# Performance work log

Measured on AMD Instinct MI355X. Metric: run time of the kernel, lower is better.

The kernel has to match this reference:

```python
import jax, jax.numpy as jnp
import numpy as np

BATCH = 4096
LATENT = 2048
ZDIM = 128
TEMP = 0.5
PRIOR = 0.3
PRIOR_PRIME = 0.5
GAMMA = 1.0
BETA = 0.0
EPS = 1e-8  # torch CosineSimilarity eps


def setup_inputs() -> dict:
    key = jax.random.key(0)
    k = jax.random.split(key, 6)
    return {
        "h_i": jax.random.normal(k[0], (BATCH, LATENT), dtype=jnp.float32),
        "h_j": jax.random.normal(k[1], (BATCH, LATENT), dtype=jnp.float32),
        "z_i": jax.random.normal(k[2], (BATCH, ZDIM), dtype=jnp.float32),
        "z_j": jax.random.normal(k[3], (BATCH, ZDIM), dtype=jnp.float32),
        "target": jax.random.randint(k[4], (BATCH, 1), 0, 2, dtype=jnp.int64 if jax.config.jax_enable_x64 else jnp.int32),
        "W": jax.random.normal(k[5], (1, LATENT), dtype=jnp.float32) * (1.0 / np.sqrt(LATENT)),
        "b": jnp.zeros((1,), dtype=jnp.float32),
        "weight_onnpu": jnp.asarray(0.5, dtype=jnp.float32),
    }


def _onnpu_loss(inp, target):
    # inp: [B, 1] classifier logit; target: [B, 1] in {0, 1} -> {-1, +1}
    t = (target * 2 - 1).astype(inp.dtype)
    positive = (t == 1).astype(inp.dtype)
    unlabeled = (t == -1).astype(inp.dtype)
    one = jnp.asarray(1.0, inp.dtype)
    n_pos = jnp.maximum(one, jnp.sum(positive))
    n_unl = jnp.maximum(one, jnp.sum(unlabeled))
    sig = jax.nn.sigmoid  # loss(x) = sigmoid(-x)
    y_pos = sig(-(positive * inp)) * positive
    y_pos_inv = sig(positive * inp) * positive
    y_unl = sig(unlabeled * inp) * unlabeled
    positive_risk = PRIOR_PRIME / n_pos * jnp.sum(y_pos)
    negative_risk = ((1.0 - PRIOR_PRIME) / (n_unl * (1.0 - PRIOR)) * jnp.sum(y_unl)
                     - (1.0 - PRIOR_PRIME) * PRIOR / (n_pos * (1.0 - PRIOR)) * jnp.sum(y_pos_inv))
    # nnPU correction (nnPU=True, beta=0, gamma=1)
    return jnp.where(negative_risk < -BETA, -GAMMA * negative_risk,
                     positive_risk + negative_risk)


def _nt_xent_loss(z_i, z_j):
    B = z_i.shape[0]
    N = 2 * B
    z = jnp.concatenate([z_i, z_j], axis=0)  # [N, D]
    zn = z / jnp.maximum(jnp.linalg.norm(z, axis=1, keepdims=True), EPS)
    sim = (zn @ zn.T) / TEMP  # [N, N] cosine similarity / temperature
    idx = jnp.arange(N)
    pos = sim[idx, (idx + B) % N]  # positive pair logit per row
    # CE over [positive | all-other-than-self]: denominator is logsumexp over
    # the row with the self-similarity (diagonal) excluded.
    sim_masked = jnp.where(idx[:, None] == idx[None, :], -jnp.inf, sim)
    lse = jax.nn.logsumexp(sim_masked, axis=1)
    return jnp.sum(lse - pos) / N


def reference(h_i, h_j, z_i, z_j, target, W, b, weight_onnpu):
    logit_i = h_i @ W.T + b  # [B, 1]
    logit_j = h_j @ W.T + b
    onnpu_l = 0.5 * (_onnpu_loss(logit_i, target) + _onnpu_loss(logit_j, target))
    nt_xent_l = _nt_xent_loss(z_i, z_j)
    return weight_onnpu * onnpu_l + (1.0 - weight_onnpu) * nt_xent_l
```

## Files before the change

### kernel.cpp

```cpp
#include <hip/hip_runtime.h>

#define BATCH  4096
#define NROWS  8192
#define LATENT 2048
#define ZDIM   128
#define PRIORc       0.3f
#define PRIOR_PRIMEc 0.5f

typedef __attribute__((ext_vector_type(8))) short bf16x8;
typedef __attribute__((ext_vector_type(4))) float f32x4;

__device__ inline unsigned short f2bf_rne(float f) {
    unsigned int u = __float_as_uint(f);
    u = u + 0x7fffu + ((u >> 16) & 1u);
    return (unsigned short)(u >> 16);
}

__device__ inline float wave_reduce_sum(float v) {
#pragma unroll
    for (int m = 1; m < 64; m <<= 1) v += __shfl_xor(v, m, 64);
    return v;
}

__global__ void k_zprep(const float* __restrict__ z_i, const float* __restrict__ z_j,
                        unsigned short* __restrict__ znb, float* __restrict__ pos) {
    int wave = threadIdx.x >> 6, lane = threadIdx.x & 63;
    int r = blockIdx.x * 4 + wave;
    int p = r + BATCH;
    float2 a = ((const float2*)(z_i + (size_t)r * ZDIM))[lane];
    float2 c = ((const float2*)(z_j + (size_t)r * ZDIM))[lane];
    float sa = a.x * a.x + a.y * a.y;
    float sc = c.x * c.x + c.y * c.y;
    float dd = a.x * c.x + a.y * c.y;
    sa = wave_reduce_sum(sa);
    sc = wave_reduce_sum(sc);
    dd = wave_reduce_sum(dd);
    float inva = 1.f / fmaxf(sqrtf(sa), 1e-8f);
    float invc = 1.f / fmaxf(sqrtf(sc), 1e-8f);
    if (lane == 0) {
        float pv = 2.0f * dd * inva * invc;
        pos[r] = pv;
        pos[p] = pv;
    }
    int kt = lane >> 4;
    int q  = (lane >> 2) & 3;
    int j  = (lane & 3) * 2;
    int lrow = q * 16;
    float fa = inva * 1.41421356237f, fc = invc * 1.41421356237f;
    {
        size_t off = ((size_t)((r >> 4) * 4 + kt) * 64 + (lrow + (r & 15))) * 8 + j;
        ushort2 w2; w2.x = f2bf_rne(a.x * fa); w2.y = f2bf_rne(a.y * fa);
        *(ushort2*)(znb + off) = w2;
    }
    {
        size_t off = ((size_t)((p >> 4) * 4 + kt) * 64 + (lrow + (p & 15))) * 8 + j;
        ushort2 w2; w2.x = f2bf_rne(c.x * fc); w2.y = f2bf_rne(c.y * fc);
        *(ushort2*)(znb + off) = w2;
    }
}

__global__ void __launch_bounds__(256, 3) k_mega(
        const unsigned short* __restrict__ znb, float* __restrict__ S_row,
        const float* __restrict__ h_i, const float* __restrict__ h_j,
        const float* __restrict__ W, const float* __restrict__ bb,
        float* __restrict__ logits) {
    int bid = blockIdx.x;
    int lane = threadIdx.x & 63, wave = threadIdx.x >> 6;
    if (bid < 1024) {
        int q = lane >> 4, t = lane & 15;
        int row0 = (bid & 63) * 128 + (wave >> 1) * 64;
        int gA = row0 >> 4;
        const bf16x8* zf = (const bf16x8*)znb;

        bf16x8 a[4][4];
#pragma unroll
        for (int mt = 0; mt < 4; ++mt)
#pragma unroll
            for (int kt = 0; kt < 4; ++kt)
                a[mt][kt] = zf[(size_t)((gA + mt) * 4 + kt) * 64 + lane];

        float s[16];
#pragma unroll
        for (int i = 0; i < 16; ++i) s[i] = 0.f;

        int colbase = (bid >> 6) * 512 + (wave & 1) * 64;
        int cb4 = colbase >> 4;
        bf16x8 b[4];
#pragma unroll
        for (int kt = 0; kt < 4; ++kt)
            b[kt] = zf[(size_t)(cb4 * 4 + kt) * 64 + lane];

#pragma unroll 1
        for (int it = 0; it < 4; ++it) {
#pragma unroll
            for (int nt = 0; nt < 4; ++nt) {
                bf16x8 bn[4];
                if (!(it == 3 && nt == 3)) {
                    int ng = cb4 + (nt == 3 ? (it + 1) * 8 : it * 8 + nt + 1);
#pragma unroll
                    for (int kt = 0; kt < 4; ++kt)
                        bn[kt] = zf[(size_t)(ng * 4 + kt) * 64 + lane];
                }
                f32x4 acc[4];
                f32x4 zero = {0.f, 0.f, 0.f, 0.f};
#pragma unroll
                for (int mt = 0; mt < 4; ++mt) acc[mt] = zero;
#pragma unroll
                for (int kt = 0; kt < 4; ++kt)
#pragma unroll
                    for (int mt = 0; mt < 4; ++mt)
                        acc[mt] = __builtin_amdgcn_mfma_f32_16x16x32_bf16(a[mt][kt], b[kt], acc[mt], 0, 0, 0);
                int gcol = colbase + it * 128 + nt * 16 + t;
#pragma unroll
                for (int mt = 0; mt < 4; ++mt) {
                    int rowb = row0 + mt * 16 + q * 4;
#pragma unroll
                    for (int reg = 0; reg < 4; ++reg) {
                        float e = __expf(acc[mt][reg]);
                        s[mt * 4 + reg] += (rowb + reg == gcol) ? 0.f : e;
                    }
                }
#pragma unroll
                for (int kt = 0; kt < 4; ++kt) b[kt] = bn[kt];
            }
        }
#pragma unroll
        for (int i = 0; i < 16; ++i) {
            float v = s[i];
            v += __shfl_xor(v, 1, 64);
            v += __shfl_xor(v, 2, 64);
            v += __shfl_xor(v, 4, 64);
            v += __shfl_xor(v, 8, 64);
            if (t == 0) atomicAdd(&S_row[row0 + (i >> 2) * 16 + q * 4 + (i & 3)], v);
        }
    } else {
        int r = (bid - 1024) * 4 + wave;
        const float* h = (r < BATCH) ? (h_i + (size_t)r * LATENT)
                                     : (h_j + (size_t)(r - BATCH) * LATENT);
        const float4* h4 = (const float4*)h;
        const float4* w4 = (const float4*)W;
        float s = 0.f;
#pragma unroll
        for (int itr = 0; itr < 8; ++itr) {
            float4 av = h4[itr * 64 + lane];
            float4 wv = w4[itr * 64 + lane];
            s += av.x * wv.x + av.y * wv.y + av.z * wv.z + av.w * wv.w;
        }
        s = wave_reduce_sum(s);
        if (lane == 0) logits[r] = s + bb[0];
    }
}

__global__ void k_final(const float* __restrict__ S_row, const float* __restrict__ pos,
                        const float* __restrict__ logits, const int* __restrict__ target,
                        const float* __restrict__ w_onnpu, float* __restrict__ out) {
    float nt_s = 0.f;
    for (int r = threadIdx.x; r < NROWS; r += 1024)
        nt_s += __logf(S_row[r]) - pos[r];
    float v[8];
#pragma unroll
    for (int i = 0; i < 8; ++i) v[i] = 0.f;
    for (int r = threadIdx.x; r < BATCH; r += 1024) {
        float li = logits[r], lj = logits[BATCH + r];
        bool p = (target[r] == 1);
        float si_n = 1.f / (1.f + __expf(li));
        float si_p = 1.f / (1.f + __expf(-li));
        float sj_n = 1.f / (1.f + __expf(lj));
        float sj_p = 1.f / (1.f + __expf(-lj));
        v[0] += p ? 1.f : 0.f;
        v[1] += p ? 0.f : 1.f;
        v[2] += p ? si_n : 0.f;
        v[3] += p ? si_p : 0.f;
        v[4] += p ? 0.f : si_p;
        v[5] += p ? sj_n : 0.f;
        v[6] += p ? sj_p : 0.f;
        v[7] += p ? 0.f : sj_p;
    }
    __shared__ float red[16][9];
    int wave = threadIdx.x >> 6, lane = threadIdx.x & 63;
    nt_s = wave_reduce_sum(nt_s);
#pragma unroll
    for (int i = 0; i < 8; ++i) v[i] = wave_reduce_sum(v[i]);
    if (lane == 0) {
        red[wave][0] = nt_s;
#pragma unroll
        for (int i = 0; i < 8; ++i) red[wave][1 + i] = v[i];
    }
    __syncthreads();
    if (threadIdx.x == 0) {
        float t[9];
#pragma unroll
        for (int i = 0; i < 9; ++i) {
            float acc = 0.f;
#pragma unroll
            for (int wv = 0; wv < 16; ++wv) acc += red[wv][i];
            t[i] = acc;
        }
        float ntxent = t[0] / (float)NROWS;
        float np = fmaxf(1.f, t[1]), nu = fmaxf(1.f, t[2]);
        float pr_i = PRIOR_PRIMEc / np * t[3];
        float nr_i = (1.f - PRIOR_PRIMEc) / (nu * (1.f - PRIORc)) * t[5]
                   - (1.f - PRIOR_PRIMEc) * PRIORc / (np * (1.f - PRIORc)) * t[4];
        float li_loss = (nr_i < 0.f) ? -nr_i : (pr_i + nr_i);
        float pr_j = PRIOR_PRIMEc / np * t[6];
        float nr_j = (1.f - PRIOR_PRIMEc) / (nu * (1.f - PRIORc)) * t[8]
                   - (1.f - PRIOR_PRIMEc) * PRIORc / (np * (1.f - PRIORc)) * t[7];
        float lj_loss = (nr_j < 0.f) ? -nr_j : (pr_j + nr_j);
        float onnpu = 0.5f * (li_loss + lj_loss);
        float w = w_onnpu[0];
        out[0] = w * onnpu + (1.f - w) * ntxent;
    }
}

extern "C" void kernel_launch(void* const* d_in, const int* in_sizes, int n_in,
                              void* d_out, int out_size, void* d_ws, size_t ws_size,
                              hipStream_t stream) {
    const float* h_i = (const float*)d_in[0];
    const float* h_j = (const float*)d_in[1];
    const float* z_i = (const float*)d_in[2];
    const float* z_j = (const float*)d_in[3];
    const int* target = (const int*)d_in[4];
    const float* W = (const float*)d_in[5];
    const float* b = (const float*)d_in[6];
    const float* w_onnpu = (const float*)d_in[7];

    char* ws = (char*)d_ws;
    unsigned short* znb = (unsigned short*)ws;
    float* S_row  = (float*)(ws + 2097152);
    float* pos    = (float*)(ws + 2097152 + 32768);
    float* logits = (float*)(ws + 2097152 + 65536);
    float* out = (float*)d_out;

    hipMemsetAsync(S_row, 0, 32768, stream);
    k_zprep<<<1024, 256, 0, stream>>>(z_i, z_j, znb, pos);
    k_mega<<<3072, 256, 0, stream>>>(znb, S_row, h_i, h_j, W, b, logits);
    k_final<<<1, 1024, 0, stream>>>(S_row, pos, logits, target, w_onnpu, out);
}
```

Before: 136.7 us.

## Use exp2 with prescaled operands, subtract diagonal term, interleave GEMM and GEMV blocks

```diff
diff --git a/kernel.cpp b/kernel.cpp
--- a/kernel.cpp
+++ b/kernel.cpp
@@ -22,19 +22,20 @@
     return v;
 }
 
+#define ZSCALE 1.69864464f
+
 __global__ void k_zprep(const float* __restrict__ z_i, const float* __restrict__ z_j,
-                        unsigned short* __restrict__ znb, float* __restrict__ pos) {
+                        unsigned short* __restrict__ znb, float* __restrict__ pos,
+                        float* __restrict__ dexp, float* __restrict__ S_row) {
+    if (threadIdx.x < 8) S_row[blockIdx.x * 8 + threadIdx.x] = 0.f;
     int wave = threadIdx.x >> 6, lane = threadIdx.x & 63;
     int r = blockIdx.x * 4 + wave;
     int p = r + BATCH;
     float2 a = ((const float2*)(z_i + (size_t)r * ZDIM))[lane];
     float2 c = ((const float2*)(z_j + (size_t)r * ZDIM))[lane];
-    float sa = a.x * a.x + a.y * a.y;
-    float sc = c.x * c.x + c.y * c.y;
-    float dd = a.x * c.x + a.y * c.y;
-    sa = wave_reduce_sum(sa);
-    sc = wave_reduce_sum(sc);
-    dd = wave_reduce_sum(dd);
+    float sa = wave_reduce_sum(a.x * a.x + a.y * a.y);
+    float sc = wave_reduce_sum(c.x * c.x + c.y * c.y);
+    float dd = wave_reduce_sum(a.x * c.x + a.y * c.y);
     float inva = 1.f / fmaxf(sqrtf(sa), 1e-8f);
     float invc = 1.f / fmaxf(sqrtf(sc), 1e-8f);
     if (lane == 0) {
@@ -46,16 +47,26 @@
     int q  = (lane >> 2) & 3;
     int j  = (lane & 3) * 2;
     int lrow = q * 16;
-    float fa = inva * 1.41421356237f, fc = invc * 1.41421356237f;
+    float fa = inva * ZSCALE, fc = invc * ZSCALE;
+    ushort2 wa; wa.x = f2bf_rne(a.x * fa); wa.y = f2bf_rne(a.y * fa);
+    ushort2 wc; wc.x = f2bf_rne(c.x * fc); wc.y = f2bf_rne(c.y * fc);
     {
         size_t off = ((size_t)((r >> 4) * 4 + kt) * 64 + (lrow + (r & 15))) * 8 + j;
-        ushort2 w2; w2.x = f2bf_rne(a.x * fa); w2.y = f2bf_rne(a.y * fa);
-        *(ushort2*)(znb + off) = w2;
+        *(ushort2*)(znb + off) = wa;
     }
     {
         size_t off = ((size_t)((p >> 4) * 4 + kt) * 64 + (lrow + (p & 15))) * 8 + j;
-        ushort2 w2; w2.x = f2bf_rne(c.x * fc); w2.y = f2bf_rne(c.y * fc);
-        *(ushort2*)(znb + off) = w2;
+        *(ushort2*)(znb + off) = wc;
+    }
+    float ax = __uint_as_float((unsigned)wa.x << 16);
+    float ay = __uint_as_float((unsigned)wa.y << 16);
+    float cx = __uint_as_float((unsigned)wc.x << 16);
+    float cy = __uint_as_float((unsigned)wc.y << 16);
+    float da = wave_reduce_sum(ax * ax + ay * ay);
+    float dc = wave_reduce_sum(cx * cx + cy * cy);
+    if (lane == 0) {
+        dexp[r] = __builtin_amdgcn_exp2f(da);
+        dexp[p] = __builtin_amdgcn_exp2f(dc);
     }
 }
 
@@ -66,9 +77,11 @@
         float* __restrict__ logits) {
     int bid = blockIdx.x;
     int lane = threadIdx.x & 63, wave = threadIdx.x >> 6;
-    if (bid < 1024) {
+    int role = bid % 3;
+    if (role == 0) {
+        int sid = bid / 3;
         int q = lane >> 4, t = lane & 15;
-        int row0 = (bid & 63) * 128 + (wave >> 1) * 64;
+        int row0 = (sid & 63) * 128 + (wave >> 1) * 64;
         int gA = row0 >> 4;
         const bf16x8* zf = (const bf16x8*)znb;
 
@@ -83,7 +96,7 @@
 #pragma unroll
         for (int i = 0; i < 16; ++i) s[i] = 0.f;
 
-        int colbase = (bid >> 6) * 512 + (wave & 1) * 64;
+        int colbase = (sid >> 6) * 512 + (wave & 1) * 64;
         int cb4 = colbase >> 4;
         bf16x8 b[4];
 #pragma unroll
@@ -110,16 +123,11 @@
 #pragma unroll
                     for (int mt = 0; mt < 4; ++mt)
                         acc[mt] = __builtin_amdgcn_mfma_f32_16x16x32_bf16(a[mt][kt], b[kt], acc[mt], 0, 0, 0);
-                int gcol = colbase + it * 128 + nt * 16 + t;
-#pragma unroll
-                for (int mt = 0; mt < 4; ++mt) {
-                    int rowb = row0 + mt * 16 + q * 4;
-#pragma unroll
-                    for (int reg = 0; reg < 4; ++reg) {
-                        float e = __expf(acc[mt][reg]);
-                        s[mt * 4 + reg] += (rowb + reg == gcol) ? 0.f : e;
-                    }
-                }
+#pragma unroll
+                for (int mt = 0; mt < 4; ++mt)
+#pragma unroll
+                    for (int reg = 0; reg < 4; ++reg)
+                        s[mt * 4 + reg] += __builtin_amdgcn_exp2f(acc[mt][reg]);
 #pragma unroll
                 for (int kt = 0; kt < 4; ++kt) b[kt] = bn[kt];
             }
@@ -134,16 +142,17 @@
             if (t == 0) atomicAdd(&S_row[row0 + (i >> 2) * 16 + q * 4 + (i & 3)], v);
         }
     } else {
-        int r = (bid - 1024) * 4 + wave;
+        int lid = (bid / 3) * 2 + (role - 1);
+        int r = lid * 4 + wave;
         const float* h = (r < BATCH) ? (h_i + (size_t)r * LATENT)
                                      : (h_j + (size_t)(r - BATCH) * LATENT);
-        const float4* h4 = (const float4*)h;
-        const float4* w4 = (const float4*)W;
+        const f32x4* h4 = (const f32x4*)h;
+        const f32x4* w4 = (const f32x4*)W;
         float s = 0.f;
 #pragma unroll
         for (int itr = 0; itr < 8; ++itr) {
-            float4 av = h4[itr * 64 + lane];
-            float4 wv = w4[itr * 64 + lane];
+            f32x4 av = __builtin_nontemporal_load(h4 + itr * 64 + lane);
+            f32x4 wv = w4[itr * 64 + lane];
             s += av.x * wv.x + av.y * wv.y + av.z * wv.z + av.w * wv.w;
         }
         s = wave_reduce_sum(s);
@@ -152,11 +161,12 @@
 }
 
 __global__ void k_final(const float* __restrict__ S_row, const float* __restrict__ pos,
-                        const float* __restrict__ logits, const int* __restrict__ target,
+                        const float* __restrict__ dexp, const float* __restrict__ logits,
+                        const int* __restrict__ target,
                         const float* __restrict__ w_onnpu, float* __restrict__ out) {
     float nt_s = 0.f;
     for (int r = threadIdx.x; r < NROWS; r += 1024)
-        nt_s += __logf(S_row[r]) - pos[r];
+        nt_s += __logf(S_row[r] - dexp[r]) - pos[r];
     float v[8];
 #pragma unroll
     for (int i = 0; i < 8; ++i) v[i] = 0.f;
@@ -229,10 +239,10 @@
     float* S_row  = (float*)(ws + 2097152);
     float* pos    = (float*)(ws + 2097152 + 32768);
     float* logits = (float*)(ws + 2097152 + 65536);
+    float* dexp   = (float*)(ws + 2097152 + 98304);
     float* out = (float*)d_out;
 
-    hipMemsetAsync(S_row, 0, 32768, stream);
-    k_zprep<<<1024, 256, 0, stream>>>(z_i, z_j, znb, pos);
+    k_zprep<<<1024, 256, 0, stream>>>(z_i, z_j, znb, pos, dexp, S_row);
     k_mega<<<3072, 256, 0, stream>>>(znb, S_row, h_i, h_j, W, b, logits);
-    k_final<<<1, 1024, 0, stream>>>(S_row, pos, logits, target, w_onnpu, out);
-}
+    k_final<<<1, 1024, 0, stream>>>(S_row, pos, dexp, logits, target, w_onnpu, out);
+}
```

Result: slower. 152.2 us (+11.3%).
